# Optimization experiments

Hardware: AMD Instinct MI355X
Metric: run time of the kernel (lower is better)

Reference implementation:

```python
import jax, jax.numpy as jnp
import numpy as np

N = 50000
E = 800000
D = 512
H = 256
K = 16
COLLAPSE_REG = 1.0


def setup_inputs() -> dict:
    key = jax.random.key(0)
    ks = jax.random.split(key, 8)
    embeddings = jax.random.normal(ks[0], (N, D), dtype=jnp.float32)
    edge_src = jax.random.randint(ks[1], (E,), 0, N, dtype=jnp.int32)
    edge_dst = jax.random.randint(ks[2], (E,), 0, N, dtype=jnp.int32)
    # GCNConv params (glorot-ish scaling)
    W1 = jax.random.normal(ks[3], (D, H), dtype=jnp.float32) / np.sqrt(D)
    b1 = jnp.zeros((H,), dtype=jnp.float32)
    W2 = jax.random.normal(ks[4], (H, H), dtype=jnp.float32) / np.sqrt(H)
    b2 = jnp.zeros((H,), dtype=jnp.float32)
    Wa = jax.random.normal(ks[5], (H, K), dtype=jnp.float32) / np.sqrt(H)
    ba = jnp.zeros((K,), dtype=jnp.float32)
    return {"embeddings": embeddings, "edge_src": edge_src, "edge_dst": edge_dst,
            "W1": W1, "b1": b1, "W2": W2, "b2": b2, "Wa": Wa, "ba": ba}


def _gcn_conv(x, W, b, src, dst, dis):
    # PyG GCNConv: transform then D^{-1/2}(A+I)D^{-1/2} aggregation + bias.
    x = x @ W                                   # [N, out]
    norm = dis[src] * dis[dst]                  # [E]
    agg = jax.ops.segment_sum(x[src] * norm[:, None], dst, num_segments=N)
    agg = agg + (dis * dis)[:, None] * x        # self-loop term
    return agg + b


def reference(embeddings, edge_src, edge_dst, W1, b1, W2, b2, Wa, ba):
    # symmetric-norm degrees with self-loops (edge weight 1)
    deg = 1.0 + jax.ops.segment_sum(jnp.ones((E,), jnp.float32), edge_dst, num_segments=N)
    dis = jax.lax.rsqrt(deg)                    # deg > 0 always (self-loop)

    x = jax.nn.selu(_gcn_conv(embeddings, W1, b1, edge_src, edge_dst, dis))
    x_skip = x  # dropout is identity in eval
    x = jax.nn.selu(_gcn_conv(x, W2, b2, edge_src, edge_dst, dis))
    x = x + x_skip
    assignments = jax.nn.softmax(x @ Wa + ba, axis=1)   # [N, K]

    # ---- DMoN losses (faithful to original, incl. scalar normalizer) ----
    degrees = jax.ops.segment_sum(jnp.ones((E,), jnp.float32), edge_src, num_segments=N)  # row sums of A
    m = degrees.sum() / 2.0
    AS = jax.ops.segment_sum(assignments[edge_dst], edge_src, num_segments=N)  # A @ S, [N, K]
    trace_pooled = jnp.sum(assignments * AS)    # trace(S^T A S)
    dS = degrees @ assignments                  # [K]
    normalizer = jnp.dot(dS, dS) / (2.0 * m)    # scalar (as in original code)
    spectral_loss = -(trace_pooled - K * normalizer) / (2.0 * m)

    cluster_sizes = assignments.sum(axis=0)     # [K]
    collapse_loss = jnp.linalg.norm(cluster_sizes) / N * jnp.sqrt(jnp.float32(K)) - 1.0
    entropy = -jnp.sum(assignments * jnp.log(assignments + 1e-8)) / N
    entropy_loss = -0.1 * entropy
    total_loss = spectral_loss + COLLAPSE_REG * collapse_loss + entropy_loss

    pooled = (assignments / (cluster_sizes + 1e-8)).T @ embeddings  # [K, D]
    return (assignments, pooled, spectral_loss, COLLAPSE_REG * collapse_loss, total_loss, entropy_loss)
```

## Files before the change

### kernel.cpp

```cpp
#include <hip/hip_runtime.h>
#include <hip/hip_fp16.h>
#include <math.h>

#define NN 50000
#define EE 800000
#define DD 512
#define HH 256
#define KK 16
#define NB_SCAN 196

typedef _Float16 half8_t __attribute__((ext_vector_type(8)));
typedef float f32x4 __attribute__((ext_vector_type(4)));

__global__ void zero_kernel(int* __restrict__ p, int n) {
    int i = blockIdx.x * blockDim.x + threadIdx.x;
    if (i < n) p[i] = 0;
}

__global__ void count_kernel(const int4* __restrict__ src4, const int4* __restrict__ dst4,
                             int* __restrict__ indeg, int* __restrict__ outdeg) {
    int e = blockIdx.x * blockDim.x + threadIdx.x;
    if (e < EE / 4) {
        int4 s = src4[e], d = dst4[e];
        atomicAdd(&outdeg[s.x], 1); atomicAdd(&outdeg[s.y], 1);
        atomicAdd(&outdeg[s.z], 1); atomicAdd(&outdeg[s.w], 1);
        atomicAdd(&indeg[d.x], 1);  atomicAdd(&indeg[d.y], 1);
        atomicAdd(&indeg[d.z], 1);  atomicAdd(&indeg[d.w], 1);
    }
}

__global__ void scan_p1(const int* __restrict__ in, int* __restrict__ part, int n,
                        const int* __restrict__ outdeg, float* __restrict__ dis,
                        float* __restrict__ degf) {
    __shared__ int tile[256];
    int t = threadIdx.x;
    int i = blockIdx.x * 256 + t;
    int v = (i < n) ? in[i] : 0;
    tile[t] = v;
    if (i < n) {
        dis[i]  = 1.0f / sqrtf(1.0f + (float)v);
        degf[i] = (float)outdeg[i];
    }
    __syncthreads();
    for (int o = 128; o > 0; o >>= 1) {
        if (t < o) tile[t] += tile[t + o];
        __syncthreads();
    }
    if (t == 0) part[blockIdx.x] = tile[0];
}

__global__ void scan_p2(int* __restrict__ part, int nb, int* __restrict__ off_end) {
    __shared__ int tile[256];
    int t = threadIdx.x;
    int v = (t < nb) ? part[t] : 0;
    tile[t] = v;
    __syncthreads();
    for (int o = 1; o < 256; o <<= 1) {
        int x = (t >= o) ? tile[t - o] : 0;
        __syncthreads();
        tile[t] += x;
        __syncthreads();
    }
    if (t < nb) part[t] = tile[t] - v;
    if (t == 255) *off_end = tile[255];
}

__global__ void scan_p3(const int* __restrict__ in, const int* __restrict__ part,
                        int* __restrict__ out, int n) {
    __shared__ int tile[256];
    int t = threadIdx.x;
    int i = blockIdx.x * 256 + t;
    int v = (i < n) ? in[i] : 0;
    tile[t] = v;
    __syncthreads();
    for (int o = 1; o < 256; o <<= 1) {
        int x = (t >= o) ? tile[t - o] : 0;
        __syncthreads();
        tile[t] += x;
        __syncthreads();
    }
    if (i < n) out[i] = part[blockIdx.x] + tile[t] - v;
}

__global__ void scatter_kernel(const int4* __restrict__ src4, const int4* __restrict__ dst4,
                               const int* __restrict__ off, int* __restrict__ cur,
                               const float* __restrict__ dis,
                               int* __restrict__ nbr, __half* __restrict__ wgt) {
    int e = blockIdx.x * blockDim.x + threadIdx.x;
    if (e < EE / 4) {
        int4 s = src4[e], d = dst4[e];
        int p, q;
        p = atomicAdd(&cur[d.x], 1); q = off[d.x] + p;
        nbr[q] = s.x; wgt[q] = __float2half(dis[s.x] * dis[d.x]);
        p = atomicAdd(&cur[d.y], 1); q = off[d.y] + p;
        nbr[q] = s.y; wgt[q] = __float2half(dis[s.y] * dis[d.y]);
        p = atomicAdd(&cur[d.z], 1); q = off[d.z] + p;
        nbr[q] = s.z; wgt[q] = __float2half(dis[s.z] * dis[d.z]);
        p = atomicAdd(&cur[d.w], 1); q = off[d.w] + p;
        nbr[q] = s.w; wgt[q] = __float2half(dis[s.w] * dis[d.w]);
    }
}

__global__ void transpose_w(const float* __restrict__ W1, __half* __restrict__ Wt1,
                            const float* __restrict__ W2, __half* __restrict__ Wt2,
                            const float* __restrict__ Wa, __half* __restrict__ WaT) {
    int i = blockIdx.x * 256 + threadIdx.x;
    if (i < DD * HH) {
        int k = i / HH, n = i % HH;
        Wt1[(size_t)n * DD + k] = __float2half(W1[i]);
    } else if (i < DD * HH + HH * HH) {
        int j = i - DD * HH;
        int k = j / HH, n = j % HH;
        Wt2[(size_t)n * HH + k] = __float2half(W2[j]);
    } else if (i < DD * HH + HH * HH + HH * KK) {
        int j = i - DD * HH - HH * HH;
        int k = j / KK, n = j % KK;
        WaT[n * HH + k] = __float2half(Wa[j]);
    }
}

__device__ inline half8_t loadfrag(const float* p) {
    float4 x0 = *(const float4*)p;
    float4 x1 = *(const float4*)(p + 4);
    half8_t h;
    h[0] = (_Float16)x0.x; h[1] = (_Float16)x0.y;
    h[2] = (_Float16)x0.z; h[3] = (_Float16)x0.w;
    h[4] = (_Float16)x1.x; h[5] = (_Float16)x1.y;
    h[6] = (_Float16)x1.z; h[7] = (_Float16)x1.w;
    return h;
}
__device__ inline half8_t loadfrag(const __half* p) { return *(const half8_t*)p; }

template <typename TA, int KDIM>
__global__ __launch_bounds__(256) void mfma_gemm(const TA* __restrict__ A,
                                                 const __half* __restrict__ Bt,
                                                 __half* __restrict__ C, int M) {
    constexpr int KI = KDIM / 32;
    int t = threadIdx.x;
    int wave = t >> 6, lane = t & 63, quad = lane >> 4, l16 = lane & 15;
    int row0 = blockIdx.x * 128, col0 = blockIdx.y * 128;
    int wm = (wave & 1) * 64, wn = (wave >> 1) * 64;

    const TA* ap[4];
    const __half* bp[4];
#pragma unroll
    for (int mi = 0; mi < 4; mi++) {
        int r = row0 + wm + mi * 16 + l16;
        if (r >= M) r = M - 1;
        ap[mi] = A + (size_t)r * KDIM + quad * 8;
    }
#pragma unroll
    for (int ni = 0; ni < 4; ni++)
        bp[ni] = Bt + (size_t)(col0 + wn + ni * 16 + l16) * KDIM + quad * 8;

    f32x4 acc[4][4] = {};
    half8_t af[4], bf[4], afn[4], bfn[4];
#pragma unroll
    for (int mi = 0; mi < 4; mi++) af[mi] = loadfrag(ap[mi]);
#pragma unroll
    for (int ni = 0; ni < 4; ni++) bf[ni] = loadfrag(bp[ni]);

#pragma unroll
    for (int i = 0; i < KI; i++) {
        if (i + 1 < KI) {
#pragma unroll
            for (int mi = 0; mi < 4; mi++) afn[mi] = loadfrag(ap[mi] + (i + 1) * 32);
#pragma unroll
            for (int ni = 0; ni < 4; ni++) bfn[ni] = loadfrag(bp[ni] + (i + 1) * 32);
        }
#pragma unroll
        for (int mi = 0; mi < 4; mi++)
#pragma unroll
            for (int ni = 0; ni < 4; ni++)
                acc[mi][ni] = __builtin_amdgcn_mfma_f32_16x16x32_f16(
                    af[mi], bf[ni], acc[mi][ni], 0, 0, 0);
        if (i + 1 < KI) {
#pragma unroll
            for (int mi = 0; mi < 4; mi++) af[mi] = afn[mi];
#pragma unroll
            for (int ni = 0; ni < 4; ni++) bf[ni] = bfn[ni];
        }
    }

#pragma unroll
    for (int mi = 0; mi < 4; mi++) {
#pragma unroll
        for (int r = 0; r < 4; r++) {
            int rr = row0 + wm + mi * 16 + quad * 4 + r;
            if (rr < M) {
#pragma unroll
                for (int ni = 0; ni < 4; ni++) {
                    C[(size_t)rr * HH + col0 + wn + ni * 16 + l16] =
                        __float2half(acc[mi][ni][r]);
                }
            }
        }
    }
}

__device__ inline void fma8(float* acc, uint4 raw, float w) {
    const __half2* h = (const __half2*)&raw;
#pragma unroll
    for (int i = 0; i < 4; i++) {
        float2 f = __half22float2(h[i]);
        acc[2 * i]     += w * f.x;
        acc[2 * i + 1] += w * f.y;
    }
}

__global__ __launch_bounds__(256) void agg_selu(const __half* __restrict__ T,
                                                const float* __restrict__ dis,
                                                const int* __restrict__ off,
                                                const int* __restrict__ nbr,
                                                const __half* __restrict__ wgt,
                                                const float* __restrict__ bias,
                                                const __half* skip, __half* out) {
    int t = threadIdx.x;
    int l32 = t & 31;
    int n = blockIdx.x * 8 + (t >> 5);
    int c = l32 * 8;
    float dn = dis[n];

    float acc[8];
#pragma unroll
    for (int i = 0; i < 8; i++) acc[i] = 0.f;
    fma8(acc, *(const uint4*)(T + (size_t)n * HH + c), dn * dn);

    int s0 = off[n], s1 = off[n + 1];
    for (int base = s0; base < s1; base += 32) {
        int cnt = min(32, s1 - base);
        int sidv = 0; float wv = 0.f;
        if (l32 < cnt) {
            sidv = nbr[base + l32];
            wv = __half2float(wgt[base + l32]);
        }
        int j = 0;
        for (; j + 8 <= cnt; j += 8) {
            int a0 = __shfl(sidv, j, 32),     a1 = __shfl(sidv, j + 1, 32);
            int a2 = __shfl(sidv, j + 2, 32), a3 = __shfl(sidv, j + 3, 32);
            int a4 = __shfl(sidv, j + 4, 32), a5 = __shfl(sidv, j + 5, 32);
            int a6 = __shfl(sidv, j + 6, 32), a7 = __shfl(sidv, j + 7, 32);
            float w0 = __shfl(wv, j, 32),     w1 = __shfl(wv, j + 1, 32);
            float w2 = __shfl(wv, j + 2, 32), w3 = __shfl(wv, j + 3, 32);
            float w4 = __shfl(wv, j + 4, 32), w5 = __shfl(wv, j + 5, 32);
            float w6 = __shfl(wv, j + 6, 32), w7 = __shfl(wv, j + 7, 32);
            uint4 r0 = *(const uint4*)(T + (size_t)a0 * HH + c);
            uint4 r1 = *(const uint4*)(T + (size_t)a1 * HH + c);
            uint4 r2 = *(const uint4*)(T + (size_t)a2 * HH + c);
            uint4 r3 = *(const uint4*)(T + (size_t)a3 * HH + c);
            uint4 r4 = *(const uint4*)(T + (size_t)a4 * HH + c);
            uint4 r5 = *(const uint4*)(T + (size_t)a5 * HH + c);
            uint4 r6 = *(const uint4*)(T + (size_t)a6 * HH + c);
            uint4 r7 = *(const uint4*)(T + (size_t)a7 * HH + c);
            fma8(acc, r0, w0); fma8(acc, r1, w1);
            fma8(acc, r2, w2); fma8(acc, r3, w3);
            fma8(acc, r4, w4); fma8(acc, r5, w5);
            fma8(acc, r6, w6); fma8(acc, r7, w7);
        }
        for (; j < cnt; j++) {
            int s = __shfl(sidv, j, 32);
            float w = __shfl(wv, j, 32);
            fma8(acc, *(const uint4*)(T + (size_t)s * HH + c), w);
        }
    }

    const float scale = 1.0507009873554805f;
    const float alpha = 1.6732632423543772f;
    float4 b0 = *(const float4*)(bias + c);
    float4 b1 = *(const float4*)(bias + c + 4);
    float bb[8] = {b0.x, b0.y, b0.z, b0.w, b1.x, b1.y, b1.z, b1.w};
    float sk8[8];
#pragma unroll
    for (int i = 0; i < 8; i++) sk8[i] = 0.f;
    if (skip) {
        uint4 raw = *(const uint4*)(skip + (size_t)n * HH + c);
        const __half2* h = (const __half2*)&raw;
#pragma unroll
        for (int i = 0; i < 4; i++) {
            float2 f = __half22float2(h[i]);
            sk8[2 * i] = f.x; sk8[2 * i + 1] = f.y;
        }
    }
    _Float16 res[8];
#pragma unroll
    for (int i = 0; i < 8; i++) {
        float v = acc[i] + bb[i];
        float r = v > 0.f ? scale * v : scale * alpha * expm1f(v);
        res[i] = (_Float16)(r + sk8[i]);
    }
    *(uint4*)(out + (size_t)n * HH + c) = *(uint4*)res;
}

__global__ __launch_bounds__(256) void assign_mfma(const __half* __restrict__ Hb,
                                                   const __half* __restrict__ WaT,
                                                   const float* __restrict__ ba,
                                                   const float* __restrict__ degf,
                                                   float* __restrict__ out_assign,
                                                   __half* __restrict__ out_f16,
                                                   float* __restrict__ scal) {
    int t = threadIdx.x;
    int wave = t >> 6, lane = t & 63, quad = lane >> 4, l16 = lane & 15;
    int nb = blockIdx.x * 256 + wave * 64;

    f32x4 acc[4] = {};
    const __half* bp = WaT + l16 * HH + quad * 8;
    const __half* ap[4];
#pragma unroll
    for (int mi = 0; mi < 4; mi++) {
        int r = nb + mi * 16 + l16;
        if (r >= NN) r = NN - 1;
        ap[mi] = Hb + (size_t)r * HH + quad * 8;
    }
#pragma unroll
    for (int s = 0; s < 8; s++) {
        half8_t bf = *(const half8_t*)(bp + s * 32);
#pragma unroll
        for (int mi = 0; mi < 4; mi++) {
            half8_t af = *(const half8_t*)(ap[mi] + s * 32);
            acc[mi] = __builtin_amdgcn_mfma_f32_16x16x32_f16(af, bf, acc[mi], 0, 0, 0);
        }
    }

    float myb = ba[l16];
    float lcs = 0.f, ldS = 0.f, lent = 0.f;
#pragma unroll
    for (int mi = 0; mi < 4; mi++) {
#pragma unroll
        for (int r = 0; r < 4; r++) {
            int node = nb + mi * 16 + quad * 4 + r;
            bool ok = node < NN;
            float logit = acc[mi][r] + myb;
            float mx = logit;
            for (int o = 1; o < 16; o <<= 1) mx = fmaxf(mx, __shfl_xor(mx, o, 16));
            float e = expf(logit - mx);
            float sum = e;
            for (int o = 1; o < 16; o <<= 1) sum += __shfl_xor(sum, o, 16);
            float a = e / sum;
            if (ok) {
                out_assign[(size_t)node * KK + l16] = a;
                out_f16[(size_t)node * KK + l16] = __float2half(a);
                lcs += a;
                ldS += degf[node] * a;
                lent += a * logf(a + 1e-8f);
            }
        }
    }
    lcs += __shfl_xor(lcs, 16); lcs += __shfl_xor(lcs, 32);
    ldS += __shfl_xor(ldS, 16); ldS += __shfl_xor(ldS, 32);
    for (int o = 32; o >= 1; o >>= 1) lent += __shfl_xor(lent, o);
    if (quad == 0) {
        atomicAdd(&scal[l16], lcs);
        atomicAdd(&scal[16 + l16], ldS);
    }
    if (lane == 0) atomicAdd(&scal[33], lent);
}

__device__ inline float dot16h(const __half* a, const __half* b) {
    uint4 a0 = *(const uint4*)a, a1 = *(const uint4*)(a + 8);
    uint4 b0 = *(const uint4*)b, b1 = *(const uint4*)(b + 8);
    float p = 0.f;
    const __half2* xa = (const __half2*)&a0;
    const __half2* xb = (const __half2*)&b0;
#pragma unroll
    for (int i = 0; i < 4; i++) {
        float2 u = __half22float2(xa[i]), v = __half22float2(xb[i]);
        p += u.x * v.x + u.y * v.y;
    }
    xa = (const __half2*)&a1; xb = (const __half2*)&b1;
#pragma unroll
    for (int i = 0; i < 4; i++) {
        float2 u = __half22float2(xa[i]), v = __half22float2(xb[i]);
        p += u.x * v.x + u.y * v.y;
    }
    return p;
}

__global__ __launch_bounds__(256) void edge_trace(const int4* __restrict__ src4,
                                                  const int4* __restrict__ dst4,
                                                  const __half* __restrict__ Ah,
                                                  float* __restrict__ scal) {
    int e = blockIdx.x * blockDim.x + threadIdx.x;
    float p = 0.f;
    if (e < EE / 4) {
        int4 s = src4[e], d = dst4[e];
        p += dot16h(Ah + (size_t)s.x * KK, Ah + (size_t)d.x * KK);
        p += dot16h(Ah + (size_t)s.y * KK, Ah + (size_t)d.y * KK);
        p += dot16h(Ah + (size_t)s.z * KK, Ah + (size_t)d.z * KK);
        p += dot16h(Ah + (size_t)s.w * KK, Ah + (size_t)d.w * KK);
    }
    for (int o = 32; o >= 1; o >>= 1) p += __shfl_xor(p, o);
    __shared__ float sp;
    if (threadIdx.x == 0) sp = 0.f;
    __syncthreads();
    if ((threadIdx.x & 63) == 0) atomicAdd(&sp, p);
    __syncthreads();
    if (threadIdx.x == 0) atomicAdd(&scal[32], sp);
}

#define PCH 125
__global__ __launch_bounds__(256) void pooled_partial(const float* __restrict__ emb,
                                                      const float* __restrict__ assign,
                                                      float* __restrict__ pool_acc) {
    int d = blockIdx.x * 256 + threadIdx.x;
    int c0 = blockIdx.y * PCH;
    float acc[KK];
#pragma unroll
    for (int k = 0; k < KK; k++) acc[k] = 0.f;
    __shared__ float sa[PCH * KK];
    {
        const float4* srcv = (const float4*)(assign + (size_t)c0 * KK);
        float4* dstv = (float4*)sa;
        for (int i = threadIdx.x; i < PCH * KK / 4; i += 256) dstv[i] = srcv[i];
    }
    __syncthreads();
    for (int j = 0; j < PCH; j++) {
        float ev = emb[(size_t)(c0 + j) * DD + d];
#pragma unroll
        for (int k4 = 0; k4 < 4; k4++) {
            float4 s4 = *(const float4*)&sa[j * KK + k4 * 4];
            acc[k4 * 4 + 0] += s4.x * ev;
            acc[k4 * 4 + 1] += s4.y * ev;
            acc[k4 * 4 + 2] += s4.z * ev;
            acc[k4 * 4 + 3] += s4.w * ev;
        }
    }
#pragma unroll
    for (int k = 0; k < KK; k++) atomicAdd(&pool_acc[k * DD + d], acc[k]);
}

__global__ void finalize(const float* __restrict__ pool_acc, const float* __restrict__ scal,
                         float* __restrict__ out) {
    int bx = blockIdx.x, t = threadIdx.x;
    if (bx < 32) {
        int i = bx * 256 + t;
        int k = i / DD;
        out[800000 + i] = pool_acc[i] / (scal[k] + 1e-8f);
    } else if (t == 0) {
        float cs2 = 0.f, ds2 = 0.f;
        for (int k = 0; k < KK; k++) {
            cs2 += scal[k] * scal[k];
            ds2 += scal[16 + k] * scal[16 + k];
        }
        float two_m = (float)EE;
        float normalizer = ds2 / two_m;
        float trace = scal[32];
        float spectral = -(trace - (float)KK * normalizer) / two_m;
        float collapse = sqrtf(cs2) / (float)NN * 4.0f - 1.0f;
        float entl = 0.1f * scal[33] / (float)NN;
        out[808192] = spectral;
        out[808193] = collapse;
        out[808194] = spectral + collapse + entl;
        out[808195] = entl;
    }
}

extern "C" void kernel_launch(void* const* d_in, const int* in_sizes, int n_in,
                              void* d_out, int out_size, void* d_ws, size_t ws_size,
                              hipStream_t stream) {
    const float* emb = (const float*)d_in[0];
    const int* esrc  = (const int*)d_in[1];
    const int* edst  = (const int*)d_in[2];
    const float* W1  = (const float*)d_in[3];
    const float* b1  = (const float*)d_in[4];
    const float* W2  = (const float*)d_in[5];
    const float* b2  = (const float*)d_in[6];
    const float* Wa  = (const float*)d_in[7];
    const float* ba  = (const float*)d_in[8];
    float* out = (float*)d_out;

    int* indeg      = (int*)d_ws;
    int* outdeg     = indeg + 50000;
    int* cur        = outdeg + 50000;
    float* pool_acc = (float*)(cur + 50000);
    float* scal     = pool_acc + 8192;
    int* part       = (int*)(scal + 64);
    int* off        = part + 256;
    int* nbr        = off + 50004;
    float* dis      = (float*)(nbr + 800000);
    float* degf     = dis + 50000;
    __half* wgt     = (__half*)(degf + 50000);
    __half* Wt1     = wgt + 800000;
    __half* Wt2     = Wt1 + 256 * 512;
    __half* WaT     = Wt2 + 256 * 256;
    __half* T       = WaT + 16 * 256;
    __half* Hb      = T + (size_t)NN * HH;
    __half* Ah      = T;

    zero_kernel<<<dim3(619), 256, 0, stream>>>((int*)d_ws, 158256);
    count_kernel<<<dim3(782), 256, 0, stream>>>((const int4*)esrc, (const int4*)edst,
                                                indeg, outdeg);

    scan_p1<<<dim3(NB_SCAN), 256, 0, stream>>>(indeg, part, NN, outdeg, dis, degf);
    scan_p2<<<dim3(1), 256, 0, stream>>>(part, NB_SCAN, off + NN);
    scan_p3<<<dim3(NB_SCAN), 256, 0, stream>>>(indeg, part, off, NN);
    scatter_kernel<<<dim3(782), 256, 0, stream>>>((const int4*)esrc, (const int4*)edst,
                                                  off, cur, dis, nbr, wgt);

    transpose_w<<<dim3(784), 256, 0, stream>>>(W1, Wt1, W2, Wt2, Wa, WaT);

    mfma_gemm<float, DD><<<dim3(392, 2), 256, 0, stream>>>(emb, Wt1, T, NN);
    agg_selu<<<dim3(6250), 256, 0, stream>>>(T, dis, off, nbr, wgt, b1, nullptr, Hb);

    mfma_gemm<__half, HH><<<dim3(392, 2), 256, 0, stream>>>(Hb, Wt2, T, NN);
    agg_selu<<<dim3(6250), 256, 0, stream>>>(T, dis, off, nbr, wgt, b2, Hb, Hb);

    assign_mfma<<<dim3(196), 256, 0, stream>>>(Hb, WaT, ba, degf, out, Ah, scal);
    edge_trace<<<dim3(782), 256, 0, stream>>>((const int4*)esrc, (const int4*)edst, Ah, scal);
    pooled_partial<<<dim3(2, 400), 256, 0, stream>>>(emb, out, pool_acc);
    finalize<<<dim3(33), 256, 0, stream>>>(pool_acc, scal, out);
}
```

Measured before the change: 618.1 us.

## Restructure GEMM tiling with shared-memory A stage; drop outdeg and edge weights

```diff
diff --git a/kernel.cpp b/kernel.cpp
--- a/kernel.cpp
+++ b/kernel.cpp
@@ -17,30 +17,23 @@
     if (i < n) p[i] = 0;
 }
 
-__global__ void count_kernel(const int4* __restrict__ src4, const int4* __restrict__ dst4,
-                             int* __restrict__ indeg, int* __restrict__ outdeg) {
+__global__ void count_kernel(const int4* __restrict__ dst4, int* __restrict__ indeg) {
     int e = blockIdx.x * blockDim.x + threadIdx.x;
     if (e < EE / 4) {
-        int4 s = src4[e], d = dst4[e];
-        atomicAdd(&outdeg[s.x], 1); atomicAdd(&outdeg[s.y], 1);
-        atomicAdd(&outdeg[s.z], 1); atomicAdd(&outdeg[s.w], 1);
-        atomicAdd(&indeg[d.x], 1);  atomicAdd(&indeg[d.y], 1);
-        atomicAdd(&indeg[d.z], 1);  atomicAdd(&indeg[d.w], 1);
+        int4 d = dst4[e];
+        atomicAdd(&indeg[d.x], 1); atomicAdd(&indeg[d.y], 1);
+        atomicAdd(&indeg[d.z], 1); atomicAdd(&indeg[d.w], 1);
     }
 }
 
 __global__ void scan_p1(const int* __restrict__ in, int* __restrict__ part, int n,
-                        const int* __restrict__ outdeg, float* __restrict__ dis,
-                        float* __restrict__ degf) {
+                        float* __restrict__ dis) {
     __shared__ int tile[256];
     int t = threadIdx.x;
     int i = blockIdx.x * 256 + t;
     int v = (i < n) ? in[i] : 0;
     tile[t] = v;
-    if (i < n) {
-        dis[i]  = 1.0f / sqrtf(1.0f + (float)v);
-        degf[i] = (float)outdeg[i];
-    }
+    if (i < n) dis[i] = 1.0f / sqrtf(1.0f + (float)v);
     __syncthreads();
     for (int o = 128; o > 0; o >>= 1) {
         if (t < o) tile[t] += tile[t + o];
@@ -84,20 +77,15 @@
 
 __global__ void scatter_kernel(const int4* __restrict__ src4, const int4* __restrict__ dst4,
                                const int* __restrict__ off, int* __restrict__ cur,
-                               const float* __restrict__ dis,
-                               int* __restrict__ nbr, __half* __restrict__ wgt) {
+                               int* __restrict__ nbr) {
     int e = blockIdx.x * blockDim.x + threadIdx.x;
     if (e < EE / 4) {
         int4 s = src4[e], d = dst4[e];
-        int p, q;
-        p = atomicAdd(&cur[d.x], 1); q = off[d.x] + p;
-        nbr[q] = s.x; wgt[q] = __float2half(dis[s.x] * dis[d.x]);
-        p = atomicAdd(&cur[d.y], 1); q = off[d.y] + p;
-        nbr[q] = s.y; wgt[q] = __float2half(dis[s.y] * dis[d.y]);
-        p = atomicAdd(&cur[d.z], 1); q = off[d.z] + p;
-        nbr[q] = s.z; wgt[q] = __float2half(dis[s.z] * dis[d.z]);
-        p = atomicAdd(&cur[d.w], 1); q = off[d.w] + p;
-        nbr[q] = s.w; wgt[q] = __float2half(dis[s.w] * dis[d.w]);
+        int p;
+        p = atomicAdd(&cur[d.x], 1); nbr[off[d.x] + p] = s.x;
+        p = atomicAdd(&cur[d.y], 1); nbr[off[d.y] + p] = s.y;
+        p = atomicAdd(&cur[d.z], 1); nbr[off[d.z] + p] = s.z;
+        p = atomicAdd(&cur[d.w], 1); nbr[off[d.w] + p] = s.w;
     }
 }
 
@@ -119,78 +107,87 @@
     }
 }
 
-__device__ inline half8_t loadfrag(const float* p) {
-    float4 x0 = *(const float4*)p;
-    float4 x1 = *(const float4*)(p + 4);
-    half8_t h;
-    h[0] = (_Float16)x0.x; h[1] = (_Float16)x0.y;
-    h[2] = (_Float16)x0.z; h[3] = (_Float16)x0.w;
-    h[4] = (_Float16)x1.x; h[5] = (_Float16)x1.y;
-    h[6] = (_Float16)x1.z; h[7] = (_Float16)x1.w;
-    return h;
-}
-__device__ inline half8_t loadfrag(const __half* p) { return *(const half8_t*)p; }
-
 template <typename TA, int KDIM>
 __global__ __launch_bounds__(256) void mfma_gemm(const TA* __restrict__ A,
                                                  const __half* __restrict__ Bt,
                                                  __half* __restrict__ C, int M) {
+    constexpr bool F32 = sizeof(TA) == 4;
+    constexpr int SROW = KDIM + 8;
     constexpr int KI = KDIM / 32;
+    constexpr int GROW = KDIM / 8;
+    constexpr int GPT = 32 * GROW / 256;
+    __shared__ _Float16 As[32 * SROW];
+
     int t = threadIdx.x;
     int wave = t >> 6, lane = t & 63, quad = lane >> 4, l16 = lane & 15;
-    int row0 = blockIdx.x * 128, col0 = blockIdx.y * 128;
-    int wm = (wave & 1) * 64, wn = (wave >> 1) * 64;
-
-    const TA* ap[4];
+    int row0 = blockIdx.x * 32;
+    int coln = wave * 64;
+
+#pragma unroll
+    for (int g = 0; g < GPT; g++) {
+        int gi = g * 256 + t;
+        int row = gi / GROW, kc = gi % GROW;
+        int grow = row0 + row;
+        if (grow >= M) grow = M - 1;
+        _Float16* dst = &As[row * SROW + kc * 8];
+        if constexpr (F32) {
+            const float* src = A + (size_t)grow * KDIM + kc * 8;
+            float4 x0 = *(const float4*)src;
+            float4 x1 = *(const float4*)(src + 4);
+            _Float16 h[8];
+            h[0] = (_Float16)x0.x; h[1] = (_Float16)x0.y;
+            h[2] = (_Float16)x0.z; h[3] = (_Float16)x0.w;
+            h[4] = (_Float16)x1.x; h[5] = (_Float16)x1.y;
+            h[6] = (_Float16)x1.z; h[7] = (_Float16)x1.w;
+            *(uint4*)dst = *(uint4*)h;
+        } else {
+            *(uint4*)dst = *(const uint4*)(A + (size_t)grow * KDIM + kc * 8);
+        }
+    }
+    __syncthreads();
+
     const __half* bp[4];
 #pragma unroll
-    for (int mi = 0; mi < 4; mi++) {
-        int r = row0 + wm + mi * 16 + l16;
-        if (r >= M) r = M - 1;
-        ap[mi] = A + (size_t)r * KDIM + quad * 8;
-    }
-#pragma unroll
     for (int ni = 0; ni < 4; ni++)
-        bp[ni] = Bt + (size_t)(col0 + wn + ni * 16 + l16) * KDIM + quad * 8;
-
-    f32x4 acc[4][4] = {};
-    half8_t af[4], bf[4], afn[4], bfn[4];
-#pragma unroll
-    for (int mi = 0; mi < 4; mi++) af[mi] = loadfrag(ap[mi]);
-#pragma unroll
-    for (int ni = 0; ni < 4; ni++) bf[ni] = loadfrag(bp[ni]);
-
-#pragma unroll
-    for (int i = 0; i < KI; i++) {
-        if (i + 1 < KI) {
-#pragma unroll
-            for (int mi = 0; mi < 4; mi++) afn[mi] = loadfrag(ap[mi] + (i + 1) * 32);
-#pragma unroll
-            for (int ni = 0; ni < 4; ni++) bfn[ni] = loadfrag(bp[ni] + (i + 1) * 32);
-        }
-#pragma unroll
-        for (int mi = 0; mi < 4; mi++)
+        bp[ni] = Bt + (size_t)(coln + ni * 16 + l16) * KDIM + quad * 8;
+
+    f32x4 acc[2][4] = {};
+    uint4 bcur[4], bnext[4];
+#pragma unroll
+    for (int ni = 0; ni < 4; ni++) bcur[ni] = *(const uint4*)bp[ni];
+
+#pragma unroll
+    for (int ki = 0; ki < KI; ki++) {
+        if (ki + 1 < KI) {
+#pragma unroll
+            for (int ni = 0; ni < 4; ni++)
+                bnext[ni] = *(const uint4*)(bp[ni] + (ki + 1) * 32);
+        }
+        half8_t af[2];
+#pragma unroll
+        for (int mi = 0; mi < 2; mi++)
+            af[mi] = *(const half8_t*)&As[(mi * 16 + l16) * SROW + ki * 32 + quad * 8];
+#pragma unroll
+        for (int mi = 0; mi < 2; mi++)
 #pragma unroll
             for (int ni = 0; ni < 4; ni++)
                 acc[mi][ni] = __builtin_amdgcn_mfma_f32_16x16x32_f16(
-                    af[mi], bf[ni], acc[mi][ni], 0, 0, 0);
-        if (i + 1 < KI) {
-#pragma unroll
-            for (int mi = 0; mi < 4; mi++) af[mi] = afn[mi];
-#pragma unroll
-            for (int ni = 0; ni < 4; ni++) bf[ni] = bfn[ni];
-        }
-    }
-
-#pragma unroll
-    for (int mi = 0; mi < 4; mi++) {
+                    af[mi], *(half8_t*)&bcur[ni], acc[mi][ni], 0, 0, 0);
+        if (ki + 1 < KI) {
+#pragma unroll
+            for (int ni = 0; ni < 4; ni++) bcur[ni] = bnext[ni];
+        }
+    }
+
+#pragma unroll
+    for (int mi = 0; mi < 2; mi++) {
 #pragma unroll
         for (int r = 0; r < 4; r++) {
-            int rr = row0 + wm + mi * 16 + quad * 4 + r;
+            int rr = row0 + mi * 16 + quad * 4 + r;
             if (rr < M) {
 #pragma unroll
                 for (int ni = 0; ni < 4; ni++) {
-                    C[(size_t)rr * HH + col0 + wn + ni * 16 + l16] =
+                    C[(size_t)rr * HH + coln + ni * 16 + l16] =
                         __float2half(acc[mi][ni][r]);
                 }
             }
@@ -212,7 +209,6 @@
                                                 const float* __restrict__ dis,
                                                 const int* __restrict__ off,
                                                 const int* __restrict__ nbr,
-                                                const __half* __restrict__ wgt,
                                                 const float* __restrict__ bias,
                                                 const __half* skip, __half* out) {
     int t = threadIdx.x;
@@ -232,7 +228,7 @@
         int sidv = 0; float wv = 0.f;
         if (l32 < cnt) {
             sidv = nbr[base + l32];
-            wv = __half2float(wgt[base + l32]);
+            wv = dis[sidv] * dn;
         }
         int j = 0;
         for (; j + 8 <= cnt; j += 8) {
@@ -294,7 +290,6 @@
 __global__ __launch_bounds__(256) void assign_mfma(const __half* __restrict__ Hb,
                                                    const __half* __restrict__ WaT,
                                                    const float* __restrict__ ba,
-                                                   const float* __restrict__ degf,
                                                    float* __restrict__ out_assign,
                                                    __half* __restrict__ out_f16,
                                                    float* __restrict__ scal) {
@@ -322,7 +317,7 @@
     }
 
     float myb = ba[l16];
-    float lcs = 0.f, ldS = 0.f, lent = 0.f;
+    float lcs = 0.f, lent = 0.f;
 #pragma unroll
     for (int mi = 0; mi < 4; mi++) {
 #pragma unroll
@@ -340,61 +335,74 @@
                 out_assign[(size_t)node * KK + l16] = a;
                 out_f16[(size_t)node * KK + l16] = __float2half(a);
                 lcs += a;
-                ldS += degf[node] * a;
                 lent += a * logf(a + 1e-8f);
             }
         }
     }
     lcs += __shfl_xor(lcs, 16); lcs += __shfl_xor(lcs, 32);
-    ldS += __shfl_xor(ldS, 16); ldS += __shfl_xor(ldS, 32);
     for (int o = 32; o >= 1; o >>= 1) lent += __shfl_xor(lent, o);
-    if (quad == 0) {
-        atomicAdd(&scal[l16], lcs);
-        atomicAdd(&scal[16 + l16], ldS);
-    }
+    if (quad == 0) atomicAdd(&scal[l16], lcs);
     if (lane == 0) atomicAdd(&scal[33], lent);
 }
 
-__device__ inline float dot16h(const __half* a, const __half* b) {
-    uint4 a0 = *(const uint4*)a, a1 = *(const uint4*)(a + 8);
-    uint4 b0 = *(const uint4*)b, b1 = *(const uint4*)(b + 8);
-    float p = 0.f;
-    const __half2* xa = (const __half2*)&a0;
-    const __half2* xb = (const __half2*)&b0;
+__device__ inline void loadrow16(const __half* p, float* v) {
+    uint4 a0 = *(const uint4*)p, a1 = *(const uint4*)(p + 8);
+    const __half2* h0 = (const __half2*)&a0;
+    const __half2* h1 = (const __half2*)&a1;
 #pragma unroll
     for (int i = 0; i < 4; i++) {
-        float2 u = __half22float2(xa[i]), v = __half22float2(xb[i]);
-        p += u.x * v.x + u.y * v.y;
-    }
-    xa = (const __half2*)&a1; xb = (const __half2*)&b1;
-#pragma unroll
-    for (int i = 0; i < 4; i++) {
-        float2 u = __half22float2(xa[i]), v = __half22float2(xb[i]);
-        p += u.x * v.x + u.y * v.y;
-    }
-    return p;
+        float2 f = __half22float2(h0[i]);
+        v[2 * i] = f.x; v[2 * i + 1] = f.y;
+        float2 g = __half22float2(h1[i]);
+        v[8 + 2 * i] = g.x; v[8 + 2 * i + 1] = g.y;
+    }
 }
 
 __global__ __launch_bounds__(256) void edge_trace(const int4* __restrict__ src4,
                                                   const int4* __restrict__ dst4,
                                                   const __half* __restrict__ Ah,
-                                                  float* __restrict__ scal) {
+                                                  float* __restrict__ scal,
+                                                  float* __restrict__ dsacc) {
     int e = blockIdx.x * blockDim.x + threadIdx.x;
+    int t = threadIdx.x;
     float p = 0.f;
+    float ds[16];
+#pragma unroll
+    for (int k = 0; k < 16; k++) ds[k] = 0.f;
     if (e < EE / 4) {
         int4 s = src4[e], d = dst4[e];
-        p += dot16h(Ah + (size_t)s.x * KK, Ah + (size_t)d.x * KK);
-        p += dot16h(Ah + (size_t)s.y * KK, Ah + (size_t)d.y * KK);
-        p += dot16h(Ah + (size_t)s.z * KK, Ah + (size_t)d.z * KK);
-        p += dot16h(Ah + (size_t)s.w * KK, Ah + (size_t)d.w * KK);
+        int ss[4] = {s.x, s.y, s.z, s.w};
+        int dd[4] = {d.x, d.y, d.z, d.w};
+#pragma unroll
+        for (int j = 0; j < 4; j++) {
+            float as_[16], ad_[16];
+            loadrow16(Ah + (size_t)ss[j] * KK, as_);
+            loadrow16(Ah + (size_t)dd[j] * KK, ad_);
+#pragma unroll
+            for (int k = 0; k < 16; k++) {
+                p += as_[k] * ad_[k];
+                ds[k] += as_[k];
+            }
+        }
     }
     for (int o = 32; o >= 1; o >>= 1) p += __shfl_xor(p, o);
+#pragma unroll
+    for (int k = 0; k < 16; k++)
+        for (int o = 32; o >= 1; o >>= 1) ds[k] += __shfl_xor(ds[k], o);
+
     __shared__ float sp;
-    if (threadIdx.x == 0) sp = 0.f;
-    __syncthreads();
-    if ((threadIdx.x & 63) == 0) atomicAdd(&sp, p);
-    __syncthreads();
-    if (threadIdx.x == 0) atomicAdd(&scal[32], sp);
+    __shared__ float sds[16];
+    if (t == 0) sp = 0.f;
+    if (t < 16) sds[t] = 0.f;
+    __syncthreads();
+    if ((t & 63) == 0) {
+        atomicAdd(&sp, p);
+#pragma unroll
+        for (int k = 0; k < 16; k++) atomicAdd(&sds[k], ds[k]);
+    }
+    __syncthreads();
+    if (t == 0) atomicAdd(&scal[32], sp);
+    if (t < 16) atomicAdd(&dsacc[t * 32], sds[t]);
 }
 
 #define PCH 125
@@ -429,7 +437,7 @@
 }
 
 __global__ void finalize(const float* __restrict__ pool_acc, const float* __restrict__ scal,
-                         float* __restrict__ out) {
+                         const float* __restrict__ dsacc, float* __restrict__ out) {
     int bx = blockIdx.x, t = threadIdx.x;
     if (bx < 32) {
         int i = bx * 256 + t;
@@ -439,7 +447,8 @@
         float cs2 = 0.f, ds2 = 0.f;
         for (int k = 0; k < KK; k++) {
             cs2 += scal[k] * scal[k];
-            ds2 += scal[16 + k] * scal[16 + k];
+            float dk = dsacc[k * 32];
+            ds2 += dk * dk;
         }
         float two_m = (float)EE;
         float normalizer = ds2 / two_m;
@@ -469,43 +478,41 @@
     float* out = (float*)d_out;
 
     int* indeg      = (int*)d_ws;
-    int* outdeg     = indeg + 50000;
-    int* cur        = outdeg + 50000;
+    int* cur        = indeg + 50000;
     float* pool_acc = (float*)(cur + 50000);
     float* scal     = pool_acc + 8192;
-    int* part       = (int*)(scal + 64);
+    float* dsacc    = scal + 64;
+    int* part       = (int*)(dsacc + 512);
     int* off        = part + 256;
     int* nbr        = off + 50004;
     float* dis      = (float*)(nbr + 800000);
-    float* degf     = dis + 50000;
-    __half* wgt     = (__half*)(degf + 50000);
-    __half* Wt1     = wgt + 800000;
+    __half* Wt1     = (__half*)(dis + 50000);
     __half* Wt2     = Wt1 + 256 * 512;
     __half* WaT     = Wt2 + 256 * 256;
     __half* T       = WaT + 16 * 256;
     __half* Hb      = T + (size_t)NN * HH;
     __half* Ah      = T;
 
-    zero_kernel<<<dim3(619), 256, 0, stream>>>((int*)d_ws, 158256);
-    count_kernel<<<dim3(782), 256, 0, stream>>>((const int4*)esrc, (const int4*)edst,
-                                                indeg, outdeg);
-
-    scan_p1<<<dim3(NB_SCAN), 256, 0, stream>>>(indeg, part, NN, outdeg, dis, degf);
+    zero_kernel<<<dim3(426), 256, 0, stream>>>((int*)d_ws, 109024);
+    count_kernel<<<dim3(782), 256, 0, stream>>>((const int4*)edst, indeg);
+
+    scan_p1<<<dim3(NB_SCAN), 256, 0, stream>>>(indeg, part, NN, dis);
     scan_p2<<<dim3(1), 256, 0, stream>>>(part, NB_SCAN, off + NN);
     scan_p3<<<dim3(NB_SCAN), 256, 0, stream>>>(indeg, part, off, NN);
     scatter_kernel<<<dim3(782), 256, 0, stream>>>((const int4*)esrc, (const int4*)edst,
-                                                  off, cur, dis, nbr, wgt);
+                                                  off, cur, nbr);
 
     transpose_w<<<dim3(784), 256, 0, stream>>>(W1, Wt1, W2, Wt2, Wa, WaT);
 
-    mfma_gemm<float, DD><<<dim3(392, 2), 256, 0, stream>>>(emb, Wt1, T, NN);
-    agg_selu<<<dim3(6250), 256, 0, stream>>>(T, dis, off, nbr, wgt, b1, nullptr, Hb);
-
-    mfma_gemm<__half, HH><<<dim3(392, 2), 256, 0, stream>>>(Hb, Wt2, T, NN);
-    agg_selu<<<dim3(6250), 256, 0, stream>>>(T, dis, off, nbr, wgt, b2, Hb, Hb);
-
-    assign_mfma<<<dim3(196), 256, 0, stream>>>(Hb, WaT, ba, degf, out, Ah, scal);
-    edge_trace<<<dim3(782), 256, 0, stream>>>((const int4*)esrc, (const int4*)edst, Ah, scal);
+    mfma_gemm<float, DD><<<dim3(1563), 256, 0, stream>>>(emb, Wt1, T, NN);
+    agg_selu<<<dim3(6250), 256, 0, stream>>>(T, dis, off, nbr, b1, nullptr, Hb);
+
+    mfma_gemm<__half, HH><<<dim3(1563), 256, 0, stream>>>(Hb, Wt2, T, NN);
+    agg_selu<<<dim3(6250), 256, 0, stream>>>(T, dis, off, nbr, b2, Hb, Hb);
+
+    assign_mfma<<<dim3(196), 256, 0, stream>>>(Hb, WaT, ba, out, Ah, scal);
+    edge_trace<<<dim3(782), 256, 0, stream>>>((const int4*)esrc, (const int4*)edst,
+                                              Ah, scal, dsacc);
     pooled_partial<<<dim3(2, 400), 256, 0, stream>>>(emb, out, pool_acc);
-    finalize<<<dim3(33), 256, 0, stream>>>(pool_acc, scal, out);
-}
+    finalize<<<dim3(33), 256, 0, stream>>>(pool_acc, scal, dsacc, out);
+}
```

New measurement: 567.5 us. 1.09x faster.
